# Kernel optimization log

Hardware: AMD Instinct MI355X
Metric: run time of the kernel (lower is better)

Reference implementation:

```python
import jax, jax.numpy as jnp
import numpy as np

EPS = 1e-05
T_ITERS = 5


def setup_inputs() -> dict:
    key = jax.random.key(0)
    x = jax.random.normal(key, (64, 64, 112, 112), dtype=jnp.float32)
    return {"x": x}


def reference(x):
    # Training-mode IterNorm (ZCA whitening via Newton-Schulz), by_instance=False.
    B, C, H, W = x.shape
    # x2: [C, m] with m = B*H*W (channels as rows, all other dims flattened)
    x2 = jnp.transpose(x, (1, 0, 2, 3)).reshape(C, -1)
    m = x2.shape[1]
    mean = jnp.mean(x2, axis=-1, keepdims=True)          # [C, 1]
    xc = x2 - mean                                        # [C, m]
    eye = jnp.eye(C, dtype=x.dtype)
    # sigma = eps*I + (1/m) xc xc^T   (torch.addmm(eps, eye, 1/m, xc, xc.T))
    sigma = EPS * eye + jnp.matmul(xc, xc.T) / m          # [C, C]
    # r_t_r = 1 / trace(sigma)
    r = 1.0 / jnp.trace(sigma)
    sigma_n = sigma * r
    p = eye
    for _ in range(T_ITERS):
        # p_{k+1} = 1.5 p_k - 0.5 p_k^3 sigma_n
        p3 = jnp.matmul(jnp.matmul(p, p), p)
        p = 1.5 * p - 0.5 * jnp.matmul(p3, sigma_n)
    wm = p * jnp.sqrt(r)                                  # whitening matrix [C, C]
    xn = jnp.matmul(wm, xc)                               # [C, m]
    Xn = jnp.transpose(xn.reshape(C, B, H, W), (1, 0, 2, 3))
    return Xn
```

## Files before the change

### kernel.cpp

```cpp
#include <hip/hip_runtime.h>

#define HW_PIX 12544
#define M_TOTAL 802816
#define TILES_PER_B 49
#define NTILE 3136
#define GRID1 784
#define EPS_IN 1e-5f

#define WS_G8   0
#define WS_S8   32768
#define WS_WM   33280
#define WS_BIAS 37376
#define WS_SG   37440

typedef __attribute__((ext_vector_type(8))) short bf16x8_t;
typedef __attribute__((ext_vector_type(4))) float f32x4_t;

__device__ __forceinline__ unsigned short f2bf(float f) {
  union { float f; unsigned u; } v; v.f = f;
  unsigned r = v.u + 0x7FFFu + ((v.u >> 16) & 1u);
  return (unsigned short)(r >> 16);
}

__device__ __forceinline__ float bf2f(unsigned short h) {
  union { unsigned u; float f; } v; v.u = ((unsigned)h) << 16;
  return v.f;
}

__global__ __launch_bounds__(256) void k_gram(const float* __restrict__ x,
                                              float* __restrict__ ws) {
  __shared__ unsigned short xs[64][264];
  __shared__ float ps[256];
  const int t    = threadIdx.x;
  const int lane = t & 63;
  const int wv   = t >> 6;
  const int bx   = blockIdx.x;

  f32x4_t acc[4];
  #pragma unroll
  for (int i = 0; i < 4; ++i) acc[i] = (f32x4_t){0.f, 0.f, 0.f, 0.f};
  float csum = 0.f;

  for (int itc = 0; itc < 4; ++itc) {
    const int ci = bx + itc * GRID1;
    const int b  = ci / TILES_PER_B;
    const int p0 = (ci - b * TILES_PER_B) * 256;
    const size_t base = (size_t)(b * 64) * HW_PIX + p0 + 4 * (t & 63);

    #pragma unroll
    for (int h = 0; h < 2; ++h) {
      float4 v[8];
      #pragma unroll
      for (int i = 0; i < 8; ++i) {
        const int c = 4 * (8 * h + i) + wv;
        v[i] = *(const float4*)(x + base + (size_t)c * HW_PIX);
      }
      #pragma unroll
      for (int i = 0; i < 8; ++i) {
        const int c = 4 * (8 * h + i) + wv;
        ushort4 hh;
        hh.x = f2bf(v[i].x); hh.y = f2bf(v[i].y);
        hh.z = f2bf(v[i].z); hh.w = f2bf(v[i].w);
        *(ushort4*)&xs[c][4 * (t & 63)] = hh;
      }
    }
    __syncthreads();

    #pragma unroll
    for (int ks = 0; ks < 8; ++ks) {
      const int col = ks * 32 + 8 * (lane >> 4);
      bf16x8_t fa = *(const bf16x8_t*)&xs[wv * 16 + (lane & 15)][col];
      #pragma unroll
      for (int cb = 0; cb < 4; ++cb) {
        bf16x8_t fb = *(const bf16x8_t*)&xs[cb * 16 + (lane & 15)][col];
        acc[cb] = __builtin_amdgcn_mfma_f32_16x16x32_bf16(fa, fb, acc[cb], 0, 0, 0);
      }
    }

    {
      const int c = t >> 2, q = t & 3;
      #pragma unroll
      for (int j = 0; j < 8; ++j) {
        bf16x8_t u = *(const bf16x8_t*)&xs[c][q * 64 + 8 * j];
        #pragma unroll
        for (int e = 0; e < 8; ++e) csum += bf2f((unsigned short)u[e]);
      }
    }
    __syncthreads();
  }

  ps[t] = csum;
  __syncthreads();
  if (t < 64) {
    float s4 = ps[4 * t] + ps[4 * t + 1] + ps[4 * t + 2] + ps[4 * t + 3];
    atomicAdd(ws + WS_S8 + (bx & 7) * 64 + t, s4);
  }
  float* G8 = ws + WS_G8 + (size_t)(bx & 7) * 4096;
  const int g = lane >> 4, cl = lane & 15;
  #pragma unroll
  for (int cb = 0; cb < 4; ++cb)
    #pragma unroll
    for (int rg = 0; rg < 4; ++rg)
      atomicAdd(&G8[(wv * 16 + g * 4 + rg) * 64 + cb * 16 + cl], acc[cb][rg]);
}

__device__ __forceinline__ void mm_core(float acc[4][4], const float (*X)[68],
                                        const float (*Y)[68], int iB, int jB) {
  #pragma unroll
  for (int a = 0; a < 4; ++a)
    #pragma unroll
    for (int b = 0; b < 4; ++b) acc[a][b] = 0.f;
  #pragma unroll 4
  for (int kq = 0; kq < 16; ++kq) {
    float4 xr[4], yr[4];
    #pragma unroll
    for (int d = 0; d < 4; ++d) {
      xr[d] = *(const float4*)&X[iB + 16 * d][4 * kq];
      yr[d] = *(const float4*)&Y[jB + 16 * d][4 * kq];
    }
    #pragma unroll
    for (int di = 0; di < 4; ++di)
      #pragma unroll
      for (int dj = 0; dj < 4; ++dj)
        acc[di][dj] += xr[di].x * yr[dj].x + xr[di].y * yr[dj].y +
                       xr[di].z * yr[dj].z + xr[di].w * yr[dj].w;
  }
}

__global__ __launch_bounds__(256) void k_ns(float* __restrict__ ws) {
  float* G8   = ws + WS_G8;
  float* S8   = ws + WS_S8;
  float* wm   = ws + WS_WM;
  float* bias = ws + WS_BIAS;
  float* Sg   = ws + WS_SG;
  __shared__ float bufs[3][64][68];
  __shared__ float mean_s[64];
  __shared__ float r_s;
  const int t = threadIdx.x;
  const float inv_m = 1.0f / (float)M_TOTAL;
  if (t < 64) {
    float s = 0.f;
    #pragma unroll
    for (int k = 0; k < 8; ++k) s += S8[k * 64 + t];
    mean_s[t] = s * inv_m;
  }
  __syncthreads();
  for (int idx = t; idx < 4096; idx += 256) {
    int i = idx >> 6, j = idx & 63;
    float g = 0.f;
    #pragma unroll
    for (int k = 0; k < 8; ++k) g += G8[k * 4096 + idx];
    bufs[1][i][j] = g * inv_m - mean_s[i] * mean_s[j] + ((i == j) ? EPS_IN : 0.f);
  }
  __syncthreads();
  if (t == 0) {
    float tr = 0.f;
    for (int i = 0; i < 64; ++i) tr += bufs[1][i][i];
    r_s = 1.0f / tr;
  }
  __syncthreads();
  const float r = r_s;
  for (int idx = t; idx < 4096; idx += 256) {
    int i = idx >> 6, j = idx & 63;
    Sg[idx] = bufs[1][i][j] * r;
    bufs[0][i][j] = (i == j) ? 1.f : 0.f;
  }
  __syncthreads();
  int pa = 0, pb = 1, pc = 2;
  const int iB = t >> 4, jB = t & 15;
  float acc[4][4];
  for (int itn = 0; itn < 5; ++itn) {
    mm_core(acc, (const float(*)[68])bufs[pa], (const float(*)[68])bufs[pa], iB, jB);
    #pragma unroll
    for (int di = 0; di < 4; ++di)
      #pragma unroll
      for (int dj = 0; dj < 4; ++dj)
        bufs[pb][iB + 16 * di][jB + 16 * dj] = acc[di][dj];
    __syncthreads();
    mm_core(acc, (const float(*)[68])bufs[pb], (const float(*)[68])bufs[pa], iB, jB);
    #pragma unroll
    for (int di = 0; di < 4; ++di)
      #pragma unroll
      for (int dj = 0; dj < 4; ++dj)
        bufs[pc][iB + 16 * di][jB + 16 * dj] = acc[di][dj];
    __syncthreads();
    for (int idx = t; idx < 4096; idx += 256)
      bufs[pb][idx >> 6][idx & 63] = Sg[idx];
    __syncthreads();
    mm_core(acc, (const float(*)[68])bufs[pc], (const float(*)[68])bufs[pb], iB, jB);
    __syncthreads();
    #pragma unroll
    for (int di = 0; di < 4; ++di)
      #pragma unroll
      for (int dj = 0; dj < 4; ++dj) {
        int ii = iB + 16 * di, jj = jB + 16 * dj;
        bufs[pc][ii][jj] = 1.5f * bufs[pa][ii][jj] - 0.5f * acc[di][dj];
      }
    __syncthreads();
    int tmp = pa; pa = pc; pc = tmp;
  }
  const float sr = sqrtf(r);
  for (int idx = t; idx < 4096; idx += 256)
    wm[idx] = bufs[pa][idx >> 6][idx & 63] * sr;
  if (t < 64) {
    float a = 0.f;
    for (int k = 0; k < 64; ++k) a += bufs[pa][t][k] * mean_s[k];
    bias[t] = -a * sr;
  }
}

__global__ __launch_bounds__(256) void k_apply(const float* __restrict__ x,
                                               const float* __restrict__ ws,
                                               float* __restrict__ out) {
  __shared__ unsigned short Y[256][68];
  const int t    = threadIdx.x;
  const int lane = t & 63;
  const int wv   = t >> 6;
  const int g    = lane >> 4;
  const int m    = lane & 15;
  const int bx   = blockIdx.x;
  const int b    = bx / TILES_PER_B;
  const int p0   = (bx - b * TILES_PER_B) * 256;
  const float* __restrict__ wm   = ws + WS_WM;
  const float* __restrict__ bias = ws + WS_BIAS;

  const int arow = wv * 16 + m;
  bf16x8_t aHi[2], aLo[2];
  #pragma unroll
  for (int ks = 0; ks < 2; ++ks) {
    #pragma unroll
    for (int e = 0; e < 8; ++e) {
      const int P = ks * 32 + g * 8 + e;
      const int c = 4 * (P & 15) + (P >> 4);
      float f = wm[arow * 64 + c];
      unsigned short hi = f2bf(f);
      unsigned short lo = f2bf(f - bf2f(hi));
      aHi[ks][e] = (short)hi;
      aLo[ks][e] = (short)lo;
    }
  }
  float bv[4];
  #pragma unroll
  for (int rr = 0; rr < 4; ++rr) bv[rr] = bias[wv * 16 + g * 4 + rr];

  const size_t gbase = (size_t)(b * 64) * HW_PIX + p0 + t;
  #pragma unroll
  for (int r = 0; r < 4; ++r) {
    float f[16];
    #pragma unroll
    for (int j = 0; j < 16; ++j)
      f[j] = x[gbase + (size_t)(4 * j + r) * HW_PIX];
    #pragma unroll
    for (int q = 0; q < 4; ++q) {
      ushort4 u;
      u.x = f2bf(f[4 * q + 0]); u.y = f2bf(f[4 * q + 1]);
      u.z = f2bf(f[4 * q + 2]); u.w = f2bf(f[4 * q + 3]);
      *(ushort4*)&Y[t][16 * r + 4 * q] = u;
    }
  }
  __syncthreads();

  const size_t obase = (size_t)(b * 64) * HW_PIX + p0;
  #pragma unroll 2
  for (int tile = 0; tile < 16; ++tile) {
    const int pcol = tile * 16 + m;
    bf16x8_t bf[2];
    #pragma unroll
    for (int ks = 0; ks < 2; ++ks) {
      union { ushort4 u2[2]; bf16x8_t v; } cu;
      cu.u2[0] = *(const ushort4*)&Y[pcol][ks * 32 + g * 8];
      cu.u2[1] = *(const ushort4*)&Y[pcol][ks * 32 + g * 8 + 4];
      bf[ks] = cu.v;
    }
    f32x4_t acc = (f32x4_t){bv[0], bv[1], bv[2], bv[3]};
    acc = __builtin_amdgcn_mfma_f32_16x16x32_bf16(aHi[0], bf[0], acc, 0, 0, 0);
    acc = __builtin_amdgcn_mfma_f32_16x16x32_bf16(aHi[1], bf[1], acc, 0, 0, 0);
    acc = __builtin_amdgcn_mfma_f32_16x16x32_bf16(aLo[0], bf[0], acc, 0, 0, 0);
    acc = __builtin_amdgcn_mfma_f32_16x16x32_bf16(aLo[1], bf[1], acc, 0, 0, 0);
    #pragma unroll
    for (int rr = 0; rr < 4; ++rr)
      out[obase + (size_t)(wv * 16 + g * 4 + rr) * HW_PIX + tile * 16 + m] = acc[rr];
  }
}

extern "C" void kernel_launch(void* const* d_in, const int* in_sizes, int n_in,
                              void* d_out, int out_size, void* d_ws, size_t ws_size,
                              hipStream_t stream) {
  const float* x = (const float*)d_in[0];
  float* out = (float*)d_out;
  float* ws  = (float*)d_ws;
  hipMemsetAsync(d_ws, 0, (32768 + 512) * sizeof(float), stream);
  k_gram<<<GRID1, 256, 0, stream>>>(x, ws);
  k_ns<<<1, 256, 0, stream>>>(ws);
  k_apply<<<NTILE, 256, 0, stream>>>(x, ws, out);
}
```

Before: 457.8 us.

## Load Gram MFMA fragments directly from global memory, skipping LDS staging

The Gram kernel no longer stages bf16 tiles in shared memory behind block barriers. Each wave now loads its own 256-pixel tile straight from global memory into MFMA fragments and computes the full 64x64 product in registers with 16 accumulators. Partial results are reduced through shared-memory atomics and then added to global memory. Channel sums are computed in fp32 before bf16 rounding. This removes the LDS round trips and barriers, in exchange for more register pressure, many shared atomics, and global loads of 32 bytes per lane that are less coalesced.

Result: slower. 547.4 us (+19.6%).

```diff
diff --git a/kernel.cpp b/kernel.cpp
--- a/kernel.cpp
+++ b/kernel.cpp
@@ -4,7 +4,6 @@
 #define M_TOTAL 802816
 #define TILES_PER_B 49
 #define NTILE 3136
-#define GRID1 784
 #define EPS_IN 1e-5f
 
 #define WS_G8   0
@@ -29,79 +28,75 @@
 
 __global__ __launch_bounds__(256) void k_gram(const float* __restrict__ x,
                                               float* __restrict__ ws) {
-  __shared__ unsigned short xs[64][264];
-  __shared__ float ps[256];
+  __shared__ float Gs[64][66];
+  __shared__ float ssum_s[64];
   const int t    = threadIdx.x;
   const int lane = t & 63;
   const int wv   = t >> 6;
+  const int g    = lane >> 4;
+  const int m    = lane & 15;
   const int bx   = blockIdx.x;
 
-  f32x4_t acc[4];
-  #pragma unroll
-  for (int i = 0; i < 4; ++i) acc[i] = (f32x4_t){0.f, 0.f, 0.f, 0.f};
-  float csum = 0.f;
-
-  for (int itc = 0; itc < 4; ++itc) {
-    const int ci = bx + itc * GRID1;
-    const int b  = ci / TILES_PER_B;
-    const int p0 = (ci - b * TILES_PER_B) * 256;
-    const size_t base = (size_t)(b * 64) * HW_PIX + p0 + 4 * (t & 63);
-
-    #pragma unroll
-    for (int h = 0; h < 2; ++h) {
-      float4 v[8];
-      #pragma unroll
-      for (int i = 0; i < 8; ++i) {
-        const int c = 4 * (8 * h + i) + wv;
-        v[i] = *(const float4*)(x + base + (size_t)c * HW_PIX);
-      }
-      #pragma unroll
-      for (int i = 0; i < 8; ++i) {
-        const int c = 4 * (8 * h + i) + wv;
-        ushort4 hh;
-        hh.x = f2bf(v[i].x); hh.y = f2bf(v[i].y);
-        hh.z = f2bf(v[i].z); hh.w = f2bf(v[i].w);
-        *(ushort4*)&xs[c][4 * (t & 63)] = hh;
-      }
-    }
-    __syncthreads();
-
-    #pragma unroll
-    for (int ks = 0; ks < 8; ++ks) {
-      const int col = ks * 32 + 8 * (lane >> 4);
-      bf16x8_t fa = *(const bf16x8_t*)&xs[wv * 16 + (lane & 15)][col];
-      #pragma unroll
-      for (int cb = 0; cb < 4; ++cb) {
-        bf16x8_t fb = *(const bf16x8_t*)&xs[cb * 16 + (lane & 15)][col];
-        acc[cb] = __builtin_amdgcn_mfma_f32_16x16x32_bf16(fa, fb, acc[cb], 0, 0, 0);
-      }
-    }
-
-    {
-      const int c = t >> 2, q = t & 3;
-      #pragma unroll
-      for (int j = 0; j < 8; ++j) {
-        bf16x8_t u = *(const bf16x8_t*)&xs[c][q * 64 + 8 * j];
-        #pragma unroll
-        for (int e = 0; e < 8; ++e) csum += bf2f((unsigned short)u[e]);
-      }
-    }
-    __syncthreads();
-  }
-
-  ps[t] = csum;
-  __syncthreads();
-  if (t < 64) {
-    float s4 = ps[4 * t] + ps[4 * t + 1] + ps[4 * t + 2] + ps[4 * t + 3];
-    atomicAdd(ws + WS_S8 + (bx & 7) * 64 + t, s4);
-  }
+  for (int i = t; i < 64 * 66; i += 256) (&Gs[0][0])[i] = 0.f;
+  if (t < 64) ssum_s[t] = 0.f;
+  __syncthreads();
+
+  const int w   = bx * 4 + wv;
+  const int b   = w / TILES_PER_B;
+  const int px0 = (w - b * TILES_PER_B) * 256;
+  const float* xb = x + (size_t)(b * 64) * HW_PIX + px0 + 8 * g;
+
+  f32x4_t acc[4][4];
+  #pragma unroll
+  for (int i = 0; i < 4; ++i)
+    #pragma unroll
+    for (int j = 0; j < 4; ++j) acc[i][j] = (f32x4_t){0.f, 0.f, 0.f, 0.f};
+  float ssum[4] = {0.f, 0.f, 0.f, 0.f};
+
+  #pragma unroll
+  for (int ks = 0; ks < 8; ++ks) {
+    bf16x8_t f[4];
+    #pragma unroll
+    for (int cb = 0; cb < 4; ++cb) {
+      const float* p = xb + (size_t)(cb * 16 + m) * HW_PIX + ks * 32;
+      float4 lo = *(const float4*)p;
+      float4 hi = *(const float4*)(p + 4);
+      ssum[cb] += (lo.x + lo.y) + (lo.z + lo.w) + (hi.x + hi.y) + (hi.z + hi.w);
+      bf16x8_t ff;
+      ff[0] = (short)f2bf(lo.x); ff[1] = (short)f2bf(lo.y);
+      ff[2] = (short)f2bf(lo.z); ff[3] = (short)f2bf(lo.w);
+      ff[4] = (short)f2bf(hi.x); ff[5] = (short)f2bf(hi.y);
+      ff[6] = (short)f2bf(hi.z); ff[7] = (short)f2bf(hi.w);
+      f[cb] = ff;
+    }
+    #pragma unroll
+    for (int ra = 0; ra < 4; ++ra)
+      #pragma unroll
+      for (int cbb = 0; cbb < 4; ++cbb)
+        acc[ra][cbb] = __builtin_amdgcn_mfma_f32_16x16x32_bf16(f[ra], f[cbb],
+                                                               acc[ra][cbb], 0, 0, 0);
+  }
+
+  #pragma unroll
+  for (int ra = 0; ra < 4; ++ra)
+    #pragma unroll
+    for (int cbb = 0; cbb < 4; ++cbb)
+      #pragma unroll
+      for (int rg = 0; rg < 4; ++rg)
+        atomicAdd(&Gs[ra * 16 + g * 4 + rg][cbb * 16 + m], acc[ra][cbb][rg]);
+  #pragma unroll
+  for (int cb = 0; cb < 4; ++cb) {
+    float v = ssum[cb];
+    v += __shfl_xor(v, 16, 64);
+    v += __shfl_xor(v, 32, 64);
+    if (g == 0) atomicAdd(&ssum_s[cb * 16 + m], v);
+  }
+  __syncthreads();
+
   float* G8 = ws + WS_G8 + (size_t)(bx & 7) * 4096;
-  const int g = lane >> 4, cl = lane & 15;
-  #pragma unroll
-  for (int cb = 0; cb < 4; ++cb)
-    #pragma unroll
-    for (int rg = 0; rg < 4; ++rg)
-      atomicAdd(&G8[(wv * 16 + g * 4 + rg) * 64 + cb * 16 + cl], acc[cb][rg]);
+  for (int i = t; i < 4096; i += 256)
+    atomicAdd(&G8[i], Gs[i >> 6][i & 63]);
+  if (t < 64) atomicAdd(ws + WS_S8 + (bx & 7) * 64 + t, ssum_s[t]);
 }
 
 __device__ __forceinline__ void mm_core(float acc[4][4], const float (*X)[68],
@@ -290,7 +285,7 @@
   float* out = (float*)d_out;
   float* ws  = (float*)d_ws;
   hipMemsetAsync(d_ws, 0, (32768 + 512) * sizeof(float), stream);
-  k_gram<<<GRID1, 256, 0, stream>>>(x, ws);
+  k_gram<<<784, 256, 0, stream>>>(x, ws);
   k_ns<<<1, 256, 0, stream>>>(ws);
   k_apply<<<NTILE, 256, 0, stream>>>(x, ws, out);
 }
```
